# Kernel tuning notes

Hardware: AMD Instinct MI355X
Metric: run time of the kernel (lower is better)

Reference implementation:

```python
import jax, jax.numpy as jnp
import numpy as np

B, S, D = 2, 4096, 512
H, DK, DV = 8, 64, 64
LN_EPS = 1e-5
ATTN_EPS = 1e-6


def layer_norm(x, g, b):
    mu = jnp.mean(x, axis=-1, keepdims=True)
    var = jnp.var(x, axis=-1, keepdims=True)
    return (x - mu) * jax.lax.rsqrt(var + LN_EPS) * g + b


def setup_inputs() -> dict:
    key = jax.random.key(0)
    ks = jax.random.split(key, 12)
    s = 1.0 / np.sqrt(D)
    inp = {
        "Q": jax.random.normal(ks[0], (B, S, D), jnp.float32),
        "K": jax.random.normal(ks[1], (B, S, D), jnp.float32),
        "V": jax.random.normal(ks[2], (B, S, D), jnp.float32),
        "W_q": jax.random.normal(ks[3], (D, H * DK), jnp.float32) * s,
        "W_k": jax.random.normal(ks[4], (D, H * DK), jnp.float32) * s,
        "W_v": jax.random.normal(ks[5], (D, H * DV), jnp.float32) * s,
        "W_o": jax.random.normal(ks[6], (H * DV, D), jnp.float32) * s,
        "ln1_g": jnp.ones((D,), jnp.float32),
        "ln1_b": jnp.zeros((D,), jnp.float32),
        "ln2_g": jnp.ones((D,), jnp.float32),
        "ln2_b": jnp.zeros((D,), jnp.float32),
        "w1": jax.random.normal(ks[7], (4 * D, D), jnp.float32) * s,  # torch Linear: (out, in)
        "b1": jnp.zeros((4 * D,), jnp.float32),
        "w2": jax.random.normal(ks[8], (D, 4 * D), jnp.float32) * (1.0 / np.sqrt(4 * D)),
        "b2": jnp.zeros((D,), jnp.float32),
    }
    return inp


def reference(Q, K, V, W_q, W_k, W_v, W_o, ln1_g, ln1_b, ln2_g, ln2_b, w1, b1, w2, b2):
    Qn = layer_norm(Q, ln1_g, ln1_b)
    # project and split heads: [B,S,H,dk] -> [B,H,S,dk]
    q = (Qn @ W_q).reshape(B, S, H, DK).transpose(0, 2, 1, 3)
    k = (K @ W_k).reshape(B, S, H, DK).transpose(0, 2, 1, 3)
    v = (V @ W_v).reshape(B, S, H, DV).transpose(0, 2, 1, 3)
    scores = jnp.einsum("bhqd,bhkd->bhqk", q, k) / (np.sqrt(DK) + ATTN_EPS)
    attn = jax.nn.softmax(scores, axis=-1)  # same as max-subtract softmax
    ctx = jnp.einsum("bhqk,bhkd->bhqd", attn, v)
    ctx = ctx.transpose(0, 2, 1, 3).reshape(B, S, H * DV)
    att_out = ctx @ W_o  # dropout = identity (eval)
    X = Q + att_out
    Xn = layer_norm(X, ln2_g, ln2_b)
    h = jax.nn.gelu(Xn @ w1.T + b1, approximate=False)
    ffn = h @ w2.T + b2
    return X + ffn
```

## Files before the change

kernel.cpp:

```cpp
#include <hip/hip_runtime.h>

typedef unsigned short u16;
typedef __attribute__((ext_vector_type(8))) short short8;
typedef __attribute__((ext_vector_type(4))) float f32x4;

struct __align__(8) us4 { u16 x, y, z, w; };
struct __align__(8) ui2 { unsigned x, y; };

#define CEXP (1.44269504089f / (8.0f + 1e-6f))

__device__ __forceinline__ u16 f2bf(float f) {
  unsigned u = __builtin_bit_cast(unsigned, f);
  unsigned r = (u + 0x7FFFu + ((u >> 16) & 1u)) >> 16;
  return (u16)r;
}

__device__ __forceinline__ unsigned pack_bf2_trunc(float a, float b) {
  return __builtin_amdgcn_perm(__builtin_bit_cast(unsigned, b),
                               __builtin_bit_cast(unsigned, a), 0x07060302u);
}

__device__ __forceinline__ void async_load16(const void* g, void* l) {
  __builtin_amdgcn_global_load_lds((const __attribute__((address_space(1))) void*)g,
                                   (__attribute__((address_space(3))) void*)l, 16, 0, 0);
}

__global__ void prep_weights(const float* __restrict__ Wq, const float* __restrict__ Wk,
                             const float* __restrict__ Wv, const float* __restrict__ Wo,
                             const float* __restrict__ w1, const float* __restrict__ w2,
                             u16* __restrict__ wqkvT, u16* __restrict__ woT,
                             u16* __restrict__ w1b, u16* __restrict__ w2b) {
  const int z = blockIdx.y;
  const int stride = gridDim.x * blockDim.x;
  const int i0 = blockIdx.x * blockDim.x + threadIdx.x;
  if (z < 4) {
    const float* src = z == 0 ? Wq : z == 1 ? Wk : z == 2 ? Wv : Wo;
    u16* dst = z < 3 ? wqkvT + z * 512 * 512 : woT;
    const float scale = (z == 0) ? CEXP : 1.0f;
    for (int i = i0; i < 512 * 512; i += stride) {
      int n = i >> 9, k = i & 511;
      dst[i] = f2bf(src[k * 512 + n] * scale);
    }
  } else {
    const float* src = z == 4 ? w1 : w2;
    u16* dst = z == 4 ? w1b : w2b;
    for (int i = i0; i < 2048 * 512; i += stride) dst[i] = f2bf(src[i]);
  }
}

template <bool KV>
__launch_bounds__(128)
__global__ void ln_cast(const float* __restrict__ X, const float* __restrict__ gw,
                        const float* __restrict__ bw, u16* __restrict__ Y,
                        const float* __restrict__ Kin, const float* __restrict__ Vin,
                        u16* __restrict__ Kb, u16* __restrict__ Vb) {
  const int row = blockIdx.x, t = threadIdx.x;
  const size_t base = (size_t)row * 512;
  float4 x = ((const float4*)(X + base))[t];
  float s = x.x + x.y + x.z + x.w;
  float ss = x.x * x.x + x.y * x.y + x.z * x.z + x.w * x.w;
#pragma unroll
  for (int off = 32; off > 0; off >>= 1) {
    s += __shfl_xor(s, off);
    ss += __shfl_xor(ss, off);
  }
  __shared__ float red[4];
  if ((t & 63) == 0) { red[(t >> 6) * 2] = s; red[(t >> 6) * 2 + 1] = ss; }
  __syncthreads();
  const float tot = red[0] + red[2], tss = red[1] + red[3];
  const float mu = tot * (1.0f / 512.0f);
  const float var = tss * (1.0f / 512.0f) - mu * mu;
  const float rs = rsqrtf(var + 1e-5f);
  float4 g4 = ((const float4*)gw)[t];
  float4 b4 = ((const float4*)bw)[t];
  us4 o;
  o.x = f2bf((x.x - mu) * rs * g4.x + b4.x);
  o.y = f2bf((x.y - mu) * rs * g4.y + b4.y);
  o.z = f2bf((x.z - mu) * rs * g4.z + b4.z);
  o.w = f2bf((x.w - mu) * rs * g4.w + b4.w);
  ((us4*)(Y + base))[t] = o;
  if constexpr (KV) {
    float4 k4 = ((const float4*)(Kin + base))[t];
    float4 v4 = ((const float4*)(Vin + base))[t];
    us4 ko, vo;
    ko.x = f2bf(k4.x); ko.y = f2bf(k4.y); ko.z = f2bf(k4.z); ko.w = f2bf(k4.w);
    vo.x = f2bf(v4.x); vo.y = f2bf(v4.y); vo.z = f2bf(v4.z); vo.w = f2bf(v4.w);
    ((us4*)(Kb + base))[t] = ko;
    ((us4*)(Vb + base))[t] = vo;
  }
}

__launch_bounds__(256, 3)
__global__ void gemm_qkv(const u16* __restrict__ Aq, const u16* __restrict__ Ak,
                         const u16* __restrict__ Av, const u16* __restrict__ Bt,
                         u16* __restrict__ qb, u16* __restrict__ kb, u16* __restrict__ vtb) {
  __shared__ __align__(16) u16 sA[128 * 32];
  __shared__ __align__(16) u16 sB[128 * 32];
  const int tid = threadIdx.x;
  const int wave = tid >> 6, lane = tid & 63;
  const int l15 = lane & 15, quad = lane >> 4;
  const int qsw = (quad ^ ((l15 >> 1) & 3)) * 8;
  const int m0 = blockIdx.x * 128, n0 = blockIdx.y * 128;
  const int sel = n0 >> 9;
  const u16* A = sel == 0 ? Aq : sel == 1 ? Ak : Av;
  const int wm = (wave >> 1) * 64, wn = (wave & 1) * 64;
  const int u0 = wave * 64 + lane, u1 = u0 + 256;
  const int sw0 = ((u0 & 3) ^ ((u0 >> 3) & 3)) * 8;
  const int K = 512;

  const u16* a0 = A + (size_t)(m0 + (u0 >> 2)) * K + sw0;
  const u16* a1 = A + (size_t)(m0 + (u1 >> 2)) * K + sw0;
  const u16* b0 = Bt + (size_t)(n0 + (u0 >> 2)) * K + sw0;
  const u16* b1p = Bt + (size_t)(n0 + (u1 >> 2)) * K + sw0;

  f32x4 acc[4][4] = {};
  for (int k0 = 0; k0 < K; k0 += 32) {
    async_load16(a0 + k0, &sA[wave * 512]);
    async_load16(a1 + k0, &sA[2048 + wave * 512]);
    async_load16(b0 + k0, &sB[wave * 512]);
    async_load16(b1p + k0, &sB[2048 + wave * 512]);
    __syncthreads();
    short8 af[4], bfr[4];
#pragma unroll
    for (int i = 0; i < 4; i++)
      af[i] = *(const short8*)&sA[(wm + i * 16 + l15) * 32 + qsw];
#pragma unroll
    for (int j = 0; j < 4; j++)
      bfr[j] = *(const short8*)&sB[(wn + j * 16 + l15) * 32 + qsw];
#pragma unroll
    for (int i = 0; i < 4; i++)
#pragma unroll
      for (int j = 0; j < 4; j++)
        acc[i][j] = __builtin_amdgcn_mfma_f32_16x16x32_bf16(af[i], bfr[j], acc[i][j], 0, 0, 0);
    __syncthreads();
  }

#pragma unroll
  for (int i = 0; i < 4; i++) {
#pragma unroll
    for (int j = 0; j < 4; j++) {
      const int ocol = ((n0 + wn) & 511) + j * 16 + l15;
      const int row0 = m0 + wm + i * 16 + quad * 4;
      if (sel < 2) {
        u16* C = sel == 0 ? qb : kb;
#pragma unroll
        for (int r = 0; r < 4; r++) C[(size_t)(row0 + r) * 512 + ocol] = f2bf(acc[i][j][r]);
      } else {
        const int b = row0 >> 12, s0 = row0 & 4095;
        const int hh = ocol >> 6, cc = ocol & 63;
        us4 pk;
        pk.x = f2bf(acc[i][j][0]); pk.y = f2bf(acc[i][j][1]);
        pk.z = f2bf(acc[i][j][2]); pk.w = f2bf(acc[i][j][3]);
        *(us4*)&vtb[((size_t)((b * 8 + hh) * 64 + cc) << 12) + s0] = pk;
      }
    }
  }
}

template <int EP, int TN, int LB>
__launch_bounds__(256, LB)
__global__ void gemm_bt(const u16* __restrict__ A, const u16* __restrict__ Bt,
                        int M, int N, int K, void* __restrict__ Cp,
                        const float* __restrict__ bias, const float* __restrict__ res) {
  constexpr int MI = (TN == 128) ? 4 : 2;
  __shared__ __align__(16) u16 sA[128 * 32];
  __shared__ __align__(16) u16 sB[TN * 32];
  const int tid = threadIdx.x;
  const int wave = tid >> 6, lane = tid & 63;
  const int l15 = lane & 15, quad = lane >> 4;
  const int qsw = (quad ^ ((l15 >> 1) & 3)) * 8;
  const int m0 = blockIdx.x * 128, n0 = blockIdx.y * TN;
  const int wm = (TN == 128) ? (wave >> 1) * 64 : wave * 32;
  const int wn = (TN == 128) ? (wave & 1) * 64 : 0;
  const int u0 = wave * 64 + lane, u1 = u0 + 256;
  const int sw0 = ((u0 & 3) ^ ((u0 >> 3) & 3)) * 8;

  const u16* a0 = A + (size_t)(m0 + (u0 >> 2)) * K + sw0;
  const u16* a1 = A + (size_t)(m0 + (u1 >> 2)) * K + sw0;
  const u16* b0 = Bt + (size_t)(n0 + (u0 >> 2)) * K + sw0;

  f32x4 acc[MI][4] = {};
  for (int k0 = 0; k0 < K; k0 += 32) {
    async_load16(a0 + k0, &sA[wave * 512]);
    async_load16(a1 + k0, &sA[2048 + wave * 512]);
    async_load16(b0 + k0, &sB[wave * 512]);
    if constexpr (TN == 128) {
      const u16* b1p = Bt + (size_t)(n0 + (u1 >> 2)) * K + sw0;
      async_load16(b1p + k0, &sB[2048 + wave * 512]);
    }
    __syncthreads();
    short8 af[MI], bfr[4];
#pragma unroll
    for (int i = 0; i < MI; i++)
      af[i] = *(const short8*)&sA[(wm + i * 16 + l15) * 32 + qsw];
#pragma unroll
    for (int j = 0; j < 4; j++)
      bfr[j] = *(const short8*)&sB[(wn + j * 16 + l15) * 32 + qsw];
#pragma unroll
    for (int i = 0; i < MI; i++)
#pragma unroll
      for (int j = 0; j < 4; j++)
        acc[i][j] = __builtin_amdgcn_mfma_f32_16x16x32_bf16(af[i], bfr[j], acc[i][j], 0, 0, 0);
    __syncthreads();
  }

#pragma unroll
  for (int i = 0; i < MI; i++) {
#pragma unroll
    for (int j = 0; j < 4; j++) {
      const int col = n0 + wn + j * 16 + l15;
      const int row0 = m0 + wm + i * 16 + quad * 4;
      if (EP == 2) {
        float* C = (float*)Cp;
#pragma unroll
        for (int r = 0; r < 4; r++) {
          size_t idx = (size_t)(row0 + r) * N + col;
          C[idx] = acc[i][j][r] + res[idx];
        }
      } else if (EP == 3) {
        u16* C = (u16*)Cp;
        const float bv = bias[col];
#pragma unroll
        for (int r = 0; r < 4; r++) {
          float xx = acc[i][j][r] + bv;
          float gl = 0.5f * xx * (1.0f + erff(xx * 0.70710678118f));
          C[(size_t)(row0 + r) * N + col] = f2bf(gl);
        }
      } else {
        float* C = (float*)Cp;
        const float bv = bias[col];
#pragma unroll
        for (int r = 0; r < 4; r++) {
          size_t idx = (size_t)(row0 + r) * N + col;
          C[idx] = acc[i][j][r] + bv + res[idx];
        }
      }
    }
  }
}

__launch_bounds__(256, 4)
__global__ void attn_kernel(const u16* __restrict__ qb, const u16* __restrict__ kb,
                            const u16* __restrict__ vtb, u16* __restrict__ ctx) {
  __shared__ __align__(16) u16 sK[2 * 128 * 32];
  __shared__ __align__(16) u16 sV[4 * 64 * 32];
  __shared__ __align__(16) u16 sP[4 * 16 * 40];
  const int tid = threadIdx.x;
  const int wave = tid >> 6, lane = tid & 63;
  const int l15 = lane & 15, quad = lane >> 4;
  const int qsw = (quad ^ ((l15 >> 1) & 3)) * 8;
  const int bh = blockIdx.y, b = bh >> 3, h = bh & 7;
  const int q0 = blockIdx.x * 64;
  const size_t rb = (size_t)b * 4096;
  const int qrow = q0 + wave * 16 + l15;

  short8 qf[2];
#pragma unroll
  for (int kk = 0; kk < 2; kk++)
    qf[kk] = *(const short8*)&qb[(rb + qrow) * 512 + h * 64 + kk * 32 + quad * 8];

  f32x4 o_t[4] = {};
  float l_part = 0.f;
  u16* myP = &sP[wave * 16 * 40];

  for (int j0 = 0; j0 < 4096; j0 += 128) {
#pragma unroll
    for (int r = 0; r < 4; r++) {
      int u = r * 256 + wave * 64 + lane;
      int kk = u >> 9, key = (u >> 2) & 127, c8 = (u & 3) ^ ((u >> 3) & 3);
      async_load16(&kb[(rb + j0 + key) * 512 + h * 64 + kk * 32 + c8 * 8],
                   &sK[(r * 256 + wave * 64) * 8]);
    }
#pragma unroll
    for (int r = 0; r < 4; r++) {
      int u = r * 256 + wave * 64 + lane;
      int kk = u >> 8, vc = (u >> 2) & 63, c8 = (u & 3) ^ ((u >> 3) & 3);
      async_load16(&vtb[((size_t)(bh * 64 + vc)) * 4096 + j0 + kk * 32 + c8 * 8],
                   &sV[(r * 256 + wave * 64) * 8]);
    }
    __syncthreads();

#pragma unroll
    for (int kk = 0; kk < 4; kk++) {
#pragma unroll
      for (int nh = 0; nh < 2; nh++) {
        const int ni = kk * 2 + nh;
        short8 af0 = *(const short8*)&sK[(ni * 16 + l15) * 32 + qsw];
        short8 af1 = *(const short8*)&sK[4096 + (ni * 16 + l15) * 32 + qsw];
        f32x4 st = {};
        st = __builtin_amdgcn_mfma_f32_16x16x32_bf16(af0, qf[0], st, 0, 0, 0);
        st = __builtin_amdgcn_mfma_f32_16x16x32_bf16(af1, qf[1], st, 0, 0, 0);
        float p0 = __builtin_amdgcn_exp2f(st[0]);
        float p1 = __builtin_amdgcn_exp2f(st[1]);
        float p2 = __builtin_amdgcn_exp2f(st[2]);
        float p3 = __builtin_amdgcn_exp2f(st[3]);
        l_part += (p0 + p1) + (p2 + p3);
        ui2 w;
        w.x = pack_bf2_trunc(p0, p1);
        w.y = pack_bf2_trunc(p2, p3);
        *(ui2*)&myP[l15 * 40 + nh * 16 + quad * 4] = w;
      }
      asm volatile("s_waitcnt lgkmcnt(0)" ::: "memory");
      short8 pf = *(const short8*)&myP[l15 * 40 + quad * 8];
      short8 vf[4];
#pragma unroll
      for (int vi = 0; vi < 4; vi++)
        vf[vi] = *(const short8*)&sV[kk * 2048 + (vi * 16 + l15) * 32 + qsw];
#pragma unroll
      for (int vi = 0; vi < 4; vi++)
        o_t[vi] = __builtin_amdgcn_mfma_f32_16x16x32_bf16(vf[vi], pf, o_t[vi], 0, 0, 0);
    }
    __syncthreads();
  }

  float l = l_part;
  l += __shfl_xor(l, 16);
  l += __shfl_xor(l, 32);
  const float inv = 1.0f / l;
#pragma unroll
  for (int vi = 0; vi < 4; vi++) {
    us4 o;
    o.x = f2bf(o_t[vi][0] * inv);
    o.y = f2bf(o_t[vi][1] * inv);
    o.z = f2bf(o_t[vi][2] * inv);
    o.w = f2bf(o_t[vi][3] * inv);
    *(us4*)&ctx[(rb + qrow) * 512 + h * 64 + vi * 16 + quad * 4] = o;
  }
}

extern "C" void kernel_launch(void* const* d_in, const int* in_sizes, int n_in,
                              void* d_out, int out_size, void* d_ws, size_t ws_size,
                              hipStream_t stream) {
  (void)in_sizes; (void)n_in; (void)out_size; (void)ws_size;
  const float* Q = (const float*)d_in[0];
  const float* K = (const float*)d_in[1];
  const float* V = (const float*)d_in[2];
  const float* W_q = (const float*)d_in[3];
  const float* W_k = (const float*)d_in[4];
  const float* W_v = (const float*)d_in[5];
  const float* W_o = (const float*)d_in[6];
  const float* ln1_g = (const float*)d_in[7];
  const float* ln1_b = (const float*)d_in[8];
  const float* ln2_g = (const float*)d_in[9];
  const float* ln2_b = (const float*)d_in[10];
  const float* w1 = (const float*)d_in[11];
  const float* b1 = (const float*)d_in[12];
  const float* w2 = (const float*)d_in[13];
  const float* b2 = (const float*)d_in[14];

  char* w = (char*)d_ws;
  const size_t MB = 1u << 20;
  u16* wqkvT = (u16*)(w);
  u16* woT = (u16*)(w + 3 * MB / 2);
  u16* w1b = (u16*)(w + 2 * MB);
  u16* w2b = (u16*)(w + 4 * MB);
  u16* Qn  = (u16*)(w + 6 * MB);
  u16* Kb  = (u16*)(w + 14 * MB);
  u16* Vb  = (u16*)(w + 22 * MB);
  u16* qb  = (u16*)(w + 30 * MB);
  u16* kb  = (u16*)(w + 38 * MB);
  u16* vtb = (u16*)(w + 46 * MB);
  u16* ctx = (u16*)(w + 54 * MB);
  float* X = (float*)(w + 62 * MB);
  u16* Xn  = (u16*)(w + 6 * MB);
  u16* hb  = (u16*)(w + 14 * MB);

  prep_weights<<<dim3(128, 6), 256, 0, stream>>>(W_q, W_k, W_v, W_o, w1, w2,
                                                 wqkvT, woT, w1b, w2b);
  ln_cast<true><<<8192, 128, 0, stream>>>(Q, ln1_g, ln1_b, Qn, K, V, Kb, Vb);
  gemm_qkv<<<dim3(64, 12), 256, 0, stream>>>(Qn, Kb, Vb, wqkvT, qb, kb, vtb);
  attn_kernel<<<dim3(64, 16), 256, 0, stream>>>(qb, kb, vtb, ctx);
  gemm_bt<2, 64, 3><<<dim3(64, 8), 256, 0, stream>>>(ctx, woT, 8192, 512, 512, X, nullptr, Q);
  ln_cast<false><<<8192, 128, 0, stream>>>(X, ln2_g, ln2_b, Xn, nullptr, nullptr, nullptr, nullptr);
  gemm_bt<3, 128, 3><<<dim3(64, 16), 256, 0, stream>>>(Xn, w1b, 8192, 2048, 512, hb, b1, nullptr);
  gemm_bt<4, 64, 3><<<dim3(64, 8), 256, 0, stream>>>(hb, w2b, 8192, 512, 2048, (float*)d_out, b2, X);
}
```

Before: 343.1 us.

## Rewrite attention with 32x32 MFMA, register P via permlane, double-buffered K/V

The attention kernel moves from 16x16x32 to 32x32x16 bf16 MFMA tiles, with 32 query rows per wave and 128 per block. The launch grid is halved to match. The softmax probabilities now go straight into the B-operand layout through permlane32_swap instead of a round trip through shared memory. K/V tiles are double-buffered so the next tile loads while the current one is computed. This is meant to cut LDS traffic, waits and per-tile synchronisation stalls, at the cost of more registers and LDS, which lowers occupancy (launch bounds 4 to 2).

```diff
diff --git a/kernel.cpp b/kernel.cpp
--- a/kernel.cpp
+++ b/kernel.cpp
@@ -3,6 +3,8 @@
 typedef unsigned short u16;
 typedef __attribute__((ext_vector_type(8))) short short8;
 typedef __attribute__((ext_vector_type(4))) float f32x4;
+typedef __attribute__((ext_vector_type(16))) float f32x16;
+typedef __attribute__((ext_vector_type(4))) unsigned u32x4;
 
 struct __align__(8) us4 { u16 x, y, z, w; };
 struct __align__(8) ui2 { unsigned x, y; };
@@ -239,92 +241,109 @@
   }
 }
 
-__launch_bounds__(256, 4)
+__launch_bounds__(256, 2)
 __global__ void attn_kernel(const u16* __restrict__ qb, const u16* __restrict__ kb,
                             const u16* __restrict__ vtb, u16* __restrict__ ctx) {
-  __shared__ __align__(16) u16 sK[2 * 128 * 32];
-  __shared__ __align__(16) u16 sV[4 * 64 * 32];
-  __shared__ __align__(16) u16 sP[4 * 16 * 40];
+  __shared__ __align__(16) u16 sK[2][128 * 64];
+  __shared__ __align__(16) u16 sV[2][64 * 128];
   const int tid = threadIdx.x;
   const int wave = tid >> 6, lane = tid & 63;
-  const int l15 = lane & 15, quad = lane >> 4;
-  const int qsw = (quad ^ ((l15 >> 1) & 3)) * 8;
+  const int l31 = lane & 31, hi = lane >> 5;
   const int bh = blockIdx.y, b = bh >> 3, h = bh & 7;
-  const int q0 = blockIdx.x * 64;
+  const int q0 = blockIdx.x * 128;
   const size_t rb = (size_t)b * 4096;
-  const int qrow = q0 + wave * 16 + l15;
-
-  short8 qf[2];
-#pragma unroll
-  for (int kk = 0; kk < 2; kk++)
-    qf[kk] = *(const short8*)&qb[(rb + qrow) * 512 + h * 64 + kk * 32 + quad * 8];
-
-  f32x4 o_t[4] = {};
+  const int qrow = q0 + wave * 32 + l31;
+
+  short8 qf[4];
+#pragma unroll
+  for (int ks = 0; ks < 4; ks++)
+    qf[ks] = *(const short8*)&qb[(rb + qrow) * 512 + h * 64 + ks * 16 + hi * 8];
+
+#define STAGE(bufidx, jj)                                                            \
+  {                                                                                  \
+    _Pragma("unroll") for (int r = 0; r < 4; r++) {                                  \
+      int u = r * 256 + wave * 64 + lane;                                            \
+      int row = u >> 3, sl = (u & 7) ^ (row & 7);                                    \
+      async_load16(&kb[(rb + (jj) + row) * 512 + h * 64 + sl * 8],                   \
+                   &sK[bufidx][(r * 256 + wave * 64) * 8]);                          \
+    }                                                                                \
+    _Pragma("unroll") for (int r = 0; r < 4; r++) {                                  \
+      int u = r * 256 + wave * 64 + lane;                                            \
+      int row = u >> 4, sl = (u & 15) ^ (row & 7);                                   \
+      async_load16(&vtb[((size_t)(bh * 64 + row)) * 4096 + (jj) + sl * 8],           \
+                   &sV[bufidx][(r * 256 + wave * 64) * 8]);                          \
+    }                                                                                \
+  }
+
+  f32x16 ov[2] = {};
   float l_part = 0.f;
-  u16* myP = &sP[wave * 16 * 40];
-
-  for (int j0 = 0; j0 < 4096; j0 += 128) {
-#pragma unroll
-    for (int r = 0; r < 4; r++) {
-      int u = r * 256 + wave * 64 + lane;
-      int kk = u >> 9, key = (u >> 2) & 127, c8 = (u & 3) ^ ((u >> 3) & 3);
-      async_load16(&kb[(rb + j0 + key) * 512 + h * 64 + kk * 32 + c8 * 8],
-                   &sK[(r * 256 + wave * 64) * 8]);
-    }
-#pragma unroll
-    for (int r = 0; r < 4; r++) {
-      int u = r * 256 + wave * 64 + lane;
-      int kk = u >> 8, vc = (u >> 2) & 63, c8 = (u & 3) ^ ((u >> 3) & 3);
-      async_load16(&vtb[((size_t)(bh * 64 + vc)) * 4096 + j0 + kk * 32 + c8 * 8],
-                   &sV[(r * 256 + wave * 64) * 8]);
-    }
-    __syncthreads();
-
-#pragma unroll
-    for (int kk = 0; kk < 4; kk++) {
-#pragma unroll
-      for (int nh = 0; nh < 2; nh++) {
-        const int ni = kk * 2 + nh;
-        short8 af0 = *(const short8*)&sK[(ni * 16 + l15) * 32 + qsw];
-        short8 af1 = *(const short8*)&sK[4096 + (ni * 16 + l15) * 32 + qsw];
-        f32x4 st = {};
-        st = __builtin_amdgcn_mfma_f32_16x16x32_bf16(af0, qf[0], st, 0, 0, 0);
-        st = __builtin_amdgcn_mfma_f32_16x16x32_bf16(af1, qf[1], st, 0, 0, 0);
-        float p0 = __builtin_amdgcn_exp2f(st[0]);
-        float p1 = __builtin_amdgcn_exp2f(st[1]);
-        float p2 = __builtin_amdgcn_exp2f(st[2]);
-        float p3 = __builtin_amdgcn_exp2f(st[3]);
-        l_part += (p0 + p1) + (p2 + p3);
-        ui2 w;
-        w.x = pack_bf2_trunc(p0, p1);
-        w.y = pack_bf2_trunc(p2, p3);
-        *(ui2*)&myP[l15 * 40 + nh * 16 + quad * 4] = w;
+
+  STAGE(0, 0);
+  asm volatile("s_waitcnt vmcnt(0)" ::: "memory");
+  __syncthreads();
+
+  for (int t = 0; t < 32; t++) {
+    const int cur = t & 1;
+    if (t < 31) STAGE(cur ^ 1, (t + 1) * 128);
+    const u16* K_ = sK[cur];
+    const u16* V_ = sV[cur];
+#pragma unroll
+    for (int kb32 = 0; kb32 < 4; kb32++) {
+      f32x16 st = {};
+#pragma unroll
+      for (int ks = 0; ks < 4; ks++) {
+        const int row = kb32 * 32 + l31;
+        const int sl = (ks * 2 + hi) ^ (row & 7);
+        short8 kf = *(const short8*)&K_[row * 64 + sl * 8];
+        st = __builtin_amdgcn_mfma_f32_32x32x16_bf16(kf, qf[ks], st, 0, 0, 0);
       }
-      asm volatile("s_waitcnt lgkmcnt(0)" ::: "memory");
-      short8 pf = *(const short8*)&myP[l15 * 40 + quad * 8];
-      short8 vf[4];
-#pragma unroll
-      for (int vi = 0; vi < 4; vi++)
-        vf[vi] = *(const short8*)&sV[kk * 2048 + (vi * 16 + l15) * 32 + qsw];
-#pragma unroll
-      for (int vi = 0; vi < 4; vi++)
-        o_t[vi] = __builtin_amdgcn_mfma_f32_16x16x32_bf16(vf[vi], pf, o_t[vi], 0, 0, 0);
-    }
-    __syncthreads();
-  }
-
-  float l = l_part;
-  l += __shfl_xor(l, 16);
-  l += __shfl_xor(l, 32);
+      float p[16];
+#pragma unroll
+      for (int i = 0; i < 16; i++) p[i] = __builtin_amdgcn_exp2f(st[i]);
+#pragma unroll
+      for (int i = 0; i < 16; i += 4)
+        l_part += (p[i] + p[i + 1]) + (p[i + 2] + p[i + 3]);
+      unsigned x0 = pack_bf2_trunc(p[0], p[1]), x1 = pack_bf2_trunc(p[2], p[3]);
+      unsigned x2 = pack_bf2_trunc(p[4], p[5]), x3 = pack_bf2_trunc(p[6], p[7]);
+      unsigned x4 = pack_bf2_trunc(p[8], p[9]), x5 = pack_bf2_trunc(p[10], p[11]);
+      unsigned x6 = pack_bf2_trunc(p[12], p[13]), x7 = pack_bf2_trunc(p[14], p[15]);
+      auto r0 = __builtin_amdgcn_permlane32_swap(x0, x2, false, false);
+      auto r1 = __builtin_amdgcn_permlane32_swap(x1, x3, false, false);
+      auto r2 = __builtin_amdgcn_permlane32_swap(x4, x6, false, false);
+      auto r3 = __builtin_amdgcn_permlane32_swap(x5, x7, false, false);
+      u32x4 w0 = {r0[0], r1[0], r0[1], r1[1]};
+      u32x4 w1 = {r2[0], r3[0], r2[1], r3[1]};
+      short8 pf0 = __builtin_bit_cast(short8, w0);
+      short8 pf1 = __builtin_bit_cast(short8, w1);
+#pragma unroll
+      for (int vb = 0; vb < 2; vb++) {
+        const int row = vb * 32 + l31;
+        const int sl0 = (kb32 * 4 + hi) ^ (row & 7);
+        const int sl1 = (kb32 * 4 + 2 + hi) ^ (row & 7);
+        short8 vf0 = *(const short8*)&V_[row * 128 + sl0 * 8];
+        short8 vf1 = *(const short8*)&V_[row * 128 + sl1 * 8];
+        ov[vb] = __builtin_amdgcn_mfma_f32_32x32x16_bf16(vf0, pf0, ov[vb], 0, 0, 0);
+        ov[vb] = __builtin_amdgcn_mfma_f32_32x32x16_bf16(vf1, pf1, ov[vb], 0, 0, 0);
+      }
+    }
+    asm volatile("s_waitcnt vmcnt(0)" ::: "memory");
+    __syncthreads();
+  }
+#undef STAGE
+
+  float l = l_part + __shfl_xor(l_part, 32);
   const float inv = 1.0f / l;
 #pragma unroll
-  for (int vi = 0; vi < 4; vi++) {
-    us4 o;
-    o.x = f2bf(o_t[vi][0] * inv);
-    o.y = f2bf(o_t[vi][1] * inv);
-    o.z = f2bf(o_t[vi][2] * inv);
-    o.w = f2bf(o_t[vi][3] * inv);
-    *(us4*)&ctx[(rb + qrow) * 512 + h * 64 + vi * 16 + quad * 4] = o;
+  for (int vb = 0; vb < 2; vb++) {
+#pragma unroll
+    for (int rg = 0; rg < 4; rg++) {
+      us4 o;
+      o.x = f2bf(ov[vb][rg * 4 + 0] * inv);
+      o.y = f2bf(ov[vb][rg * 4 + 1] * inv);
+      o.z = f2bf(ov[vb][rg * 4 + 2] * inv);
+      o.w = f2bf(ov[vb][rg * 4 + 3] * inv);
+      *(us4*)&ctx[(rb + qrow) * 512 + h * 64 + vb * 32 + rg * 8 + hi * 4] = o;
+    }
   }
 }
 
@@ -369,7 +388,7 @@
                                                  wqkvT, woT, w1b, w2b);
   ln_cast<true><<<8192, 128, 0, stream>>>(Q, ln1_g, ln1_b, Qn, K, V, Kb, Vb);
   gemm_qkv<<<dim3(64, 12), 256, 0, stream>>>(Qn, Kb, Vb, wqkvT, qb, kb, vtb);
-  attn_kernel<<<dim3(64, 16), 256, 0, stream>>>(qb, kb, vtb, ctx);
+  attn_kernel<<<dim3(32, 16), 256, 0, stream>>>(qb, kb, vtb, ctx);
   gemm_bt<2, 64, 3><<<dim3(64, 8), 256, 0, stream>>>(ctx, woT, 8192, 512, 512, X, nullptr, Q);
   ln_cast<false><<<8192, 128, 0, stream>>>(X, ln2_g, ln2_b, Xn, nullptr, nullptr, nullptr, nullptr);
   gemm_bt<3, 128, 3><<<dim3(64, 16), 256, 0, stream>>>(Xn, w1b, 8192, 2048, 512, hb, b1, nullptr);
```

Result: faster. 335.5 us (-2.2%).
